# Kernel optimization log

Hardware: AMD Instinct MI355X
Metric: run time of the kernel (lower is better)

The kernel has to match this reference:

```python
import jax, jax.numpy as jnp
import numpy as np

B, SEQ, NNODES = 4, 12, 1024
SEG_LEN, SEG_NUM = 3, 4
HID, FF, DK, NH, NLAYERS = 64, 2048, 32, 8, 2


def setup_inputs() -> dict:
    key = jax.random.key(0)
    ks = iter(jax.random.split(key, 64))
    def nrm(shape, scale=0.05):
        return jax.random.normal(next(ks), shape, dtype=jnp.float32) * scale
    ones = lambda s: jnp.ones(s, jnp.float32)
    zeros = lambda s: jnp.zeros(s, jnp.float32)
    S, L = 2, NLAYERS
    return {
        'traffic': nrm((B, SEQ, NNODES), 1.0),
        'user': nrm((B, SEQ, NNODES), 1.0),
        'patch_w': nrm((S, HID, SEG_LEN)), 'patch_b': nrm((S, HID)),
        'mha_w': nrm((S, L, 3 * HID, HID)), 'mha_b': nrm((S, L, 3 * HID)),
        'out_w': nrm((S, L, HID, HID)), 'out_b': nrm((S, L, HID)),
        'ff1_w': nrm((S, L, FF, HID)), 'ff1_b': nrm((S, L, FF)),
        'ff2_w': nrm((S, L, HID, FF)), 'ff2_b': nrm((S, L, HID)),
        'ln1_g': ones((S, L, HID)), 'ln1_b': zeros((S, L, HID)),
        'ln2_g': ones((S, L, HID)), 'ln2_b': zeros((S, L, HID)),
        'ga_wq': nrm((S, L, DK, HID)), 'ga_wk': nrm((S, L, DK, HID)), 'ga_wv': nrm((S, L, HID, HID)),
        'ga_ff1_w': nrm((S, L, FF, HID)), 'ga_ff1_b': nrm((S, L, FF)),
        'ga_ff2_w': nrm((S, L, HID, FF)), 'ga_ff2_b': nrm((S, L, HID)),
        'ga_ln1_g': ones((S, L, HID)), 'ga_ln1_b': zeros((S, L, HID)),
        'ga_ln2_g': ones((S, L, HID)), 'ga_ln2_b': zeros((S, L, HID)),
        'ca_wq': nrm((DK, 2 * HID)), 'ca_wk': nrm((DK, 2 * HID)), 'ca_wv': nrm((HID, 2 * HID)),
    }


def _ln(x, g, b, eps=1e-5):
    m = x.mean(-1, keepdims=True)
    v = jnp.mean((x - m) ** 2, -1, keepdims=True)
    return (x - m) / jnp.sqrt(v + eps) * g + b


def _pe(s, d):
    pos = jnp.arange(s, dtype=jnp.float32)[:, None]
    div = jnp.exp(jnp.arange(0, d, 2, dtype=jnp.float32) * (-np.log(10000.0) / d))
    pe = jnp.zeros((s, d), jnp.float32)
    pe = pe.at[:, 0::2].set(jnp.sin(pos * div))
    pe = pe.at[:, 1::2].set(jnp.cos(pos * div))
    return pe


def _mha(x, w, b, wo, bo):
    # standard nn.MultiheadAttention self-attn, batch_first; x: [B,S,H]
    qkv = x @ w.T + b
    q, k, v = jnp.split(qkv, 3, axis=-1)
    def heads(t):
        b_, s_, h_ = t.shape
        return t.reshape(b_, s_, NH, h_ // NH).transpose(0, 2, 1, 3)
    q, k, v = heads(q), heads(k), heads(v)
    scale = 1.0 / jnp.sqrt(jnp.float32(HID // NH))
    att = jax.nn.softmax(jnp.einsum('bhqd,bhkd->bhqk', q, k) * scale, axis=-1)
    o = jnp.einsum('bhqk,bhkd->bhqd', att, v).transpose(0, 2, 1, 3).reshape(x.shape)
    return o @ wo.T + bo


def _enc_layer(x, p):
    # TransformerEncoderLayer_cross, post-norm, dropout=0 (eval)
    x = _ln(x + _mha(x, p['mw'], p['mb'], p['ow'], p['ob']), p['g1'], p['b1'])
    f = jax.nn.relu(x @ p['f1w'].T + p['f1b']) @ p['f2w'].T + p['f2b']
    return _ln(x + f, p['g2'], p['b2'])


def _graph_att(x, p):
    # GraphAttention.forward (bias=None, mask=None, dropout=0)
    q = x @ p['wq'].T
    k = x @ p['wk'].T
    v = x @ p['wv'].T
    dist = jax.nn.softmax(jnp.einsum('bnd,bmd->bnm', q, k) / jnp.sqrt(jnp.float32(DK)), axis=-1)
    att = jnp.einsum('bnm,bmd->bnd', dist, v)
    att = _ln(att, p['g1'], p['b1']) + x
    f = jax.nn.relu(att @ p['f1w'].T + p['f1b']) @ p['f2w'].T + p['f2b']
    return _ln(att + f, p['g2'], p['b2'])


def reference(traffic, user, patch_w, patch_b, mha_w, mha_b, out_w, out_b,
              ff1_w, ff1_b, ff2_w, ff2_b, ln1_g, ln1_b, ln2_g, ln2_b,
              ga_wq, ga_wk, ga_wv, ga_ff1_w, ga_ff1_b, ga_ff2_w, ga_ff2_b,
              ga_ln1_g, ga_ln1_b, ga_ln2_g, ga_ln2_b, ca_wq, ca_wk, ca_wv):
    pe = _pe(SEG_NUM, HID)

    def encode(x, s):
        b, _, d = x.shape
        # DSW_embedding: b (seg_num seg_len) d -> b d seg_num seg_len, then Linear
        seg = x.reshape(b, SEG_NUM, SEG_LEN, d).transpose(0, 3, 1, 2)
        z = seg @ patch_w[s].T + patch_b[s]          # [b, d, seg_num, HID]
        z = z + pe                                    # positional encoding over patches
        for i in range(NLAYERS):
            # temporal attention over the patch axis
            zt = z.reshape(b * d, SEG_NUM, HID)
            zt = _enc_layer(zt, dict(mw=mha_w[s, i], mb=mha_b[s, i], ow=out_w[s, i], ob=out_b[s, i],
                                     f1w=ff1_w[s, i], f1b=ff1_b[s, i], f2w=ff2_w[s, i], f2b=ff2_b[s, i],
                                     g1=ln1_g[s, i], b1=ln1_b[s, i], g2=ln2_g[s, i], b2=ln2_b[s, i]))
            z = zt.reshape(b, d, SEG_NUM, HID)
            # spatial graph attention over the node axis
            zs = z.transpose(0, 2, 1, 3).reshape(b * SEG_NUM, d, HID)
            zs = _graph_att(zs, dict(wq=ga_wq[s, i], wk=ga_wk[s, i], wv=ga_wv[s, i],
                                     f1w=ga_ff1_w[s, i], f1b=ga_ff1_b[s, i], f2w=ga_ff2_w[s, i], f2b=ga_ff2_b[s, i],
                                     g1=ga_ln1_g[s, i], b1=ga_ln1_b[s, i], g2=ga_ln2_g[s, i], b2=ga_ln2_b[s, i]))
            z = zs.reshape(b, SEG_NUM, d, HID).transpose(0, 2, 1, 3)
        return z.mean(axis=2)                         # pool patches -> [b, d, HID]

    enc = jnp.concatenate([encode(traffic, 0), encode(user, 1)], axis=-1)  # [b, d, 2*HID]
    # encoder_attn: SelfAttention(2*HID -> dim_k=32, dim_v=HID)
    q = enc @ ca_wq.T
    k = enc @ ca_wk.T
    v = enc @ ca_wv.T
    dist = jax.nn.softmax(jnp.einsum('bnd,bmd->bnm', q, k) / jnp.sqrt(jnp.float32(DK)), axis=-1)
    return jnp.einsum('bnm,bmd->bnd', dist, v)        # [b, n_nodes, HID]
```

## Files before the change

kernel.cpp:

```cpp
#include <hip/hip_runtime.h>
#include <hip/hip_bf16.h>
#include <math.h>

#define BB 4
#define SEQL 12
#define NN 1024
#define SEGL 3
#define SEGN 4
#define HID 64
#define FFD 2048
#define DKK 32
#define NHH 8
#define HDD 8
#define ZS 1048576

using bf16 = __hip_bfloat16;
__device__ __forceinline__ float b2f(bf16 v) { return __bfloat162float(v); }

typedef __attribute__((ext_vector_type(8))) short s8v;
typedef __attribute__((ext_vector_type(4))) float f4v;
typedef __attribute__((ext_vector_type(4))) unsigned short u4v;

__device__ __forceinline__ unsigned short f2b(float f) {
  bf16 h = __float2bfloat16(f);
  unsigned short u; __builtin_memcpy(&u, &h, 2); return u;
}
__device__ __forceinline__ float us2f(unsigned short u) {
  unsigned int e = ((unsigned int)u) << 16;
  float f; __builtin_memcpy(&f, &e, 4); return f;
}

template <int F>
__device__ __forceinline__ float ldw(const void* p, long i) {
  if (F) return ((const float*)p)[i];
  return b2f(((const bf16*)p)[i]);
}
template <int F>
__device__ __forceinline__ s8v ldfrag(const void* p, long elemOff) {
  if (F) {
    const float* fp = (const float*)p + elemOff;
    f4v u = *(const f4v*)fp, v = *(const f4v*)(fp + 4);
    s8v t;
    t[0]=f2b(u[0]); t[1]=f2b(u[1]); t[2]=f2b(u[2]); t[3]=f2b(u[3]);
    t[4]=f2b(v[0]); t[5]=f2b(v[1]); t[6]=f2b(v[2]); t[7]=f2b(v[3]);
    return t;
  }
  return *(const s8v*)((const unsigned short*)p + elemOff);
}
template <int F>
__device__ __forceinline__ f4v ldb4(const void* p, long i) {
  if (F) return *(const f4v*)((const float*)p + i);
  u4v u = *(const u4v*)((const unsigned short*)p + i);
  f4v r; r[0]=us2f(u[0]); r[1]=us2f(u[1]); r[2]=us2f(u[2]); r[3]=us2f(u[3]);
  return r;
}

__global__ void k_zero(unsigned short* __restrict__ o, int n) {
  int i = blockIdx.x * 256 + threadIdx.x;
  if (i < n) o[i] = 0;
}

__global__ void k_detect(const void* __restrict__ x0, int* __restrict__ flag) {
  int t = threadIdx.x;
  int bad = 0;
  const bf16* p = (const bf16*)x0;
  for (int i = t; i < 512; i += 256) {
    float a = fabsf(b2f(p[i]));
    if (!(a < 1e4f) || (a != 0.f && a < 1e-4f)) bad = 1;
  }
  __shared__ int tot;
  if (t == 0) tot = 0;
  __syncthreads();
  unsigned long long m = __ballot(bad);
  if ((t & 63) == 0) atomicAdd(&tot, __popcll(m));
  __syncthreads();
  if (t == 0) *flag = (tot > 64) ? 1 : 0;
}

template <int F>
__device__ __forceinline__ void wconv_body(const void* __restrict__ w1,
    const void* __restrict__ w2, const void* __restrict__ w3,
    const void* __restrict__ w4, unsigned short* __restrict__ out) {
  int i = blockIdx.x * 256 + threadIdx.x;
  long e8 = (long)i * 8;
  int slot = (int)(e8 >> 17);
  int si = slot >> 2, which = slot & 3;
  long r = e8 & 131071;
  const void* src = (which == 0) ? w1 : (which == 1) ? w2 : (which == 2) ? w3 : w4;
  *(s8v*)(out + e8) = ldfrag<F>(src, (long)si*FFD*HID + r);
}
__global__ __launch_bounds__(256) void k_wconv(const void* w1, const void* w2,
    const void* w3, const void* w4, unsigned short* out,
    const int* __restrict__ flag) {
  if (*flag) wconv_body<1>(w1, w2, w3, w4, out);
  else       wconv_body<0>(w1, w2, w3, w4, out);
}

template <int F>
__device__ __forceinline__ void patch_body(const void* __restrict__ xt,
    const void* __restrict__ xu,
    const void* __restrict__ pw, const void* __restrict__ pb,
    float* __restrict__ z) {
  int bid = blockIdx.x;
  int s = bid >> 12, rem = bid & 4095;
  int b = rem >> 10, n = rem & 1023;
  const void* x = s ? xu : xt;
  long opw = (long)s*HID*SEGL, opb = (long)s*HID;
  int g = threadIdx.x >> 6, h = threadIdx.x & 63;
  float acc = ldw<F>(pb, opb + h);
#pragma unroll
  for (int l = 0; l < SEGL; ++l)
    acc += ldw<F>(x, (long)(b*SEQL + g*SEGL + l)*NN + n) * ldw<F>(pw, opw + h*SEGL + l);
  int i2 = h >> 1;
  float dv = expf((float)(2*i2) * (-logf(10000.f) / (float)HID));
  float ang = (float)g * dv;
  acc += (h & 1) ? cosf(ang) : sinf(ang);
  z[(long)s*ZS + ((long)(b*NN + n)*SEGN + g)*HID + h] = acc;
}
__global__ __launch_bounds__(256) void k_patch(const void* __restrict__ xt,
    const void* __restrict__ xu,
    const void* __restrict__ pw, const void* __restrict__ pb,
    float* __restrict__ z, const int* __restrict__ flag) {
  if (*flag) patch_body<1>(xt, xu, pw, pb, z);
  else       patch_body<0>(xt, xu, pw, pb, z);
}

#define TT 64
#define FRW 64
#define HCS 74

__device__ __forceinline__ void ff_ld(const unsigned short* __restrict__ wc1,
    const unsigned short* __restrict__ wc2, int hb, int srow, int le,
    s8v* r1, s8v* r2) {
  r1[0] = *(const s8v*)(wc1 + (long)(hb + srow)*HID + le*8);
  r1[1] = *(const s8v*)(wc1 + (long)(hb + srow + 8)*HID + le*8);
  r2[0] = *(const s8v*)(wc2 + (long)srow*FFD + hb + le*8);
  r2[1] = *(const s8v*)(wc2 + (long)(srow + 8)*FFD + hb + le*8);
}
__device__ __forceinline__ void ff_wr(char* ldsbuf, int pb, int srow, int swb,
    const s8v* r1, const s8v* r2) {
  char* w1b = ldsbuf + pb*8192;
  char* w2b = ldsbuf + 16384 + pb*8192;
  *(s8v*)(w1b + srow*128 + swb) = r1[0];
  *(s8v*)(w1b + (srow + 8)*128 + swb) = r1[1];
  *(s8v*)(w2b + srow*128 + swb) = r2[0];
  *(s8v*)(w2b + (srow + 8)*128 + swb) = r2[1];
}

template <int F>
__device__ __forceinline__ void tff_body(float* __restrict__ zb,
    const void* __restrict__ W, const void* __restrict__ bq,
    const void* __restrict__ WO, const void* __restrict__ bo,
    const void* __restrict__ g1, const void* __restrict__ b1,
    const unsigned short* __restrict__ wcw, int li,
    const void* __restrict__ B1, const void* __restrict__ B2,
    const void* __restrict__ G, const void* __restrict__ Bt,
    char* lds) {
  int s = blockIdx.x >> 8, blk = blockIdx.x & 255;
  long si = s*2 + li;
  float* z = zb + (long)s*ZS;
  long oW = si*3*HID*HID, obq = si*3*HID, oWO = si*HID*HID, obo = si*HID;
  long og1 = si*HID, ob1 = si*HID;
  const unsigned short* wc1 = wcw + (si*4 + 0)*131072;
  const unsigned short* wc2 = wcw + (si*4 + 1)*131072;
  long fob1 = si*FFD, fob2 = si*HID, fog = si*HID, fobt = si*HID;
  unsigned short (*qkvs)[200] = (unsigned short(*)[200])lds;
  unsigned short (*ao)[72]    = (unsigned short(*)[72])(lds + 25600);
  float (*yb)[68]             = (float(*)[68])(lds + 34816);
  int tid = threadIdx.x;
  int w = tid >> 6, lane = tid & 63;
  int col = lane & 15, quad = lane >> 4;
  long r0 = (long)blk * TT;
  float* stashW = (float*)(lds + 59648 + w*4352);

  int lr = lane >> 3, le = lane & 7;
  int srow = w*16 + lr;
  int swb = ((le ^ lr) << 4);
  s8v cw1[2], cw2[2];
  ff_ld(wc1, wc2, 0, srow, le, cw1, cw2);

  s8v bx[4][2];
#pragma unroll
  for (int mt = 0; mt < 4; ++mt) {
    const float* xr = z + (r0 + mt*16 + col) * HID;
#pragma unroll
    for (int ks = 0; ks < 2; ++ks) {
      const float* p = xr + ks*32 + quad*8;
      f4v u = *(const f4v*)p, v = *(const f4v*)(p + 4);
      s8v t;
      t[0]=f2b(u[0]); t[1]=f2b(u[1]); t[2]=f2b(u[2]); t[3]=f2b(u[3]);
      t[4]=f2b(v[0]); t[5]=f2b(v[1]); t[6]=f2b(v[2]); t[7]=f2b(v[3]);
      bx[mt][ks] = t;
    }
  }
#pragma unroll
  for (int nt = 0; nt < 3; ++nt) {
    int cbase = (w*3 + nt) * 16;
    s8v aw[2];
#pragma unroll
    for (int ks = 0; ks < 2; ++ks)
      aw[ks] = ldfrag<F>(W, oW + (long)(cbase + col)*HID + ks*32 + quad*8);
    f4v bv = ldb4<F>(bq, obq + cbase + quad*4);
#pragma unroll
    for (int mt = 0; mt < 4; ++mt) {
      f4v sv = (f4v){0.f,0.f,0.f,0.f};
#pragma unroll
      for (int ks = 0; ks < 2; ++ks)
        sv = __builtin_amdgcn_mfma_f32_16x16x32_bf16(aw[ks], bx[mt][ks], sv, 0, 0, 0);
      unsigned short pk[4];
#pragma unroll
      for (int r = 0; r < 4; ++r) pk[r] = f2b(sv[r] + bv[r]);
      *(unsigned long long*)&qkvs[mt*16 + col][cbase + quad*4] =
        (unsigned long long)pk[0] | ((unsigned long long)pk[1] << 16) |
        ((unsigned long long)pk[2] << 32) | ((unsigned long long)pk[3] << 48);
    }
  }
  __syncthreads();
  if (tid < 128) {
    int gi = tid >> 3, hd = tid & 7;
    int tl = gi * 4;
    float qv[4][8], kv[4][8], vv[4][8];
#pragma unroll
    for (int t4 = 0; t4 < 4; ++t4) {
      s8v qq = *(const s8v*)&qkvs[tl + t4][hd*8];
      s8v kk = *(const s8v*)&qkvs[tl + t4][64 + hd*8];
      s8v vq = *(const s8v*)&qkvs[tl + t4][128 + hd*8];
#pragma unroll
      for (int e = 0; e < 8; ++e) {
        qv[t4][e] = us2f((unsigned short)qq[e]);
        kv[t4][e] = us2f((unsigned short)kk[e]);
        vv[t4][e] = us2f((unsigned short)vq[e]);
      }
    }
    const float sc8 = 0.3535533905932738f;
#pragma unroll
    for (int qt = 0; qt < 4; ++qt) {
      float sc[4]; float mx = -1e30f;
#pragma unroll
      for (int kt = 0; kt < 4; ++kt) {
        float d = 0;
#pragma unroll
        for (int e = 0; e < 8; ++e) d += qv[qt][e]*kv[kt][e];
        sc[kt] = d*sc8; mx = fmaxf(mx, sc[kt]);
      }
      float se = 0;
#pragma unroll
      for (int kt = 0; kt < 4; ++kt) { sc[kt] = expf(sc[kt]-mx); se += sc[kt]; }
      float inv = 1.f/se;
      s8v outp;
#pragma unroll
      for (int e = 0; e < 8; ++e) {
        float o = 0;
#pragma unroll
        for (int kt = 0; kt < 4; ++kt) o += sc[kt]*vv[kt][e];
        outp[e] = (short)f2b(o*inv);
      }
      *(s8v*)&ao[tl + qt][hd*8] = outp;
    }
  }
  __syncthreads();
  s8v awo[2];
#pragma unroll
  for (int ks = 0; ks < 2; ++ks)
    awo[ks] = ldfrag<F>(WO, oWO + (long)(w*16 + col)*HID + ks*32 + quad*8);
  f4v bov = ldb4<F>(bo, obo + w*16 + quad*4);
#pragma unroll
  for (int mt = 0; mt < 4; ++mt) {
    f4v ov = (f4v){0.f,0.f,0.f,0.f};
#pragma unroll
    for (int ks = 0; ks < 2; ++ks) {
      s8v bao = *(const s8v*)&ao[mt*16 + col][ks*32 + quad*8];
      ov = __builtin_amdgcn_mfma_f32_16x16x32_bf16(awo[ks], bao, ov, 0, 0, 0);
    }
    f4v yv;
#pragma unroll
    for (int r = 0; r < 4; ++r) yv[r] = ov[r] + bov[r];
    *(f4v*)&yb[mt*16 + col][w*16 + quad*4] = yv;
  }
  __syncthreads();
  {
    float gg = ldw<F>(g1, og1 + lane), bb2 = ldw<F>(b1, ob1 + lane);
#pragma unroll
    for (int rr = 0; rr < 16; ++rr) {
      int row = w*16 + rr;
      long tok = r0 + row;
      float val = yb[row][lane] + z[tok*HID + lane];
      float sm = val;
#pragma unroll
      for (int off = 32; off; off >>= 1) sm += __shfl_xor(sm, off);
      float m = sm*(1.f/HID);
      float d = val - m, sq = d*d;
#pragma unroll
      for (int off = 32; off; off >>= 1) sq += __shfl_xor(sq, off);
      float rv = rsqrtf(sq*(1.f/HID) + 1e-5f);
      stashW[rr*68 + lane] = d*rv*gg + bb2;
    }
  }
  __syncthreads();

  unsigned short* hcw = (unsigned short*)(lds + 32768 + w*2368);
  float* red = (float*)(lds + 42240 + w*4352);

  s8v bx2[2];
#pragma unroll
  for (int ks = 0; ks < 2; ++ks) {
    const float* p = &stashW[col*68 + ks*32 + quad*8];
    f4v u = *(const f4v*)p, v = *(const f4v*)(p + 4);
    s8v t;
    t[0]=f2b(u[0]); t[1]=f2b(u[1]); t[2]=f2b(u[2]); t[3]=f2b(u[3]);
    t[4]=f2b(v[0]); t[5]=f2b(v[1]); t[6]=f2b(v[2]); t[7]=f2b(v[3]);
    bx2[ks] = t;
  }

  f4v acc[4];
#pragma unroll
  for (int m = 0; m < 4; ++m) acc[m] = (f4v){0.f,0.f,0.f,0.f};

  ff_wr(lds, 0, srow, swb, cw1, cw2);
  __syncthreads();

  const int sw = (col & 7) << 4;
  s8v nw1[2], nw2[2];
  for (int c = 0; c < 32; ++c) {
    int pb = c & 1;
    if (c < 31) ff_ld(wc1, wc2, (c+1)*64, srow, le, nw1, nw2);
    const char* w1b = lds + pb*8192;
    const char* w2b = lds + 16384 + pb*8192;
    const int hb = c*64;
#pragma unroll
    for (int t = 0; t < 4; ++t) {
      int row = t*16 + col;
      s8v a10 = *(const s8v*)(w1b + row*128 + ((quad*16) ^ sw));
      s8v a11 = *(const s8v*)(w1b + row*128 + ((64 + quad*16) ^ sw));
      f4v bv = ldb4<F>(B1, fob1 + hb + t*16 + quad*4);
      f4v sv = __builtin_amdgcn_mfma_f32_16x16x32_bf16(a10, bx2[0],
                 (f4v){0.f,0.f,0.f,0.f}, 0, 0, 0);
      sv = __builtin_amdgcn_mfma_f32_16x16x32_bf16(a11, bx2[1], sv, 0, 0, 0);
      unsigned short pk[4];
#pragma unroll
      for (int r = 0; r < 4; ++r) pk[r] = f2b(fmaxf(sv[r] + bv[r], 0.f));
      *(unsigned long long*)&hcw[col*HCS + t*16 + quad*4] =
        (unsigned long long)pk[0] | ((unsigned long long)pk[1] << 16) |
        ((unsigned long long)pk[2] << 32) | ((unsigned long long)pk[3] << 48);
    }
#pragma unroll
    for (int ks2 = 0; ks2 < 2; ++ks2) {
      s8v bh = *(const s8v*)&hcw[col*HCS + ks2*32 + quad*8];
#pragma unroll
      for (int m = 0; m < 4; ++m) {
        int r2 = m*16 + col;
        s8v a2 = *(const s8v*)(w2b + r2*128 + ((ks2*64 + quad*16) ^ sw));
        acc[m] = __builtin_amdgcn_mfma_f32_16x16x32_bf16(a2, bh, acc[m], 0, 0, 0);
      }
    }
    if (c < 31) ff_wr(lds, pb ^ 1, srow, swb, nw1, nw2);
    __syncthreads();
  }

#pragma unroll
  for (int m = 0; m < 4; ++m)
    *(f4v*)&red[col*68 + m*16 + quad*4] = acc[m];
  float fgg = ldw<F>(G, fog + lane), fbbt = ldw<F>(Bt, fobt + lane);
  float b2v = ldw<F>(B2, fob2 + lane);
#pragma unroll
  for (int rr = 0; rr < 16; ++rr) {
    long grow = r0 + w*16 + rr;
    float val = red[rr*68 + lane] + b2v + stashW[rr*68 + lane];
    float sm = val;
#pragma unroll
    for (int off = 32; off; off >>= 1) sm += __shfl_xor(sm, off);
    float m = sm * (1.f/HID);
    float d = val - m;
    float sq = d*d;
#pragma unroll
    for (int off = 32; off; off >>= 1) sq += __shfl_xor(sq, off);
    float rv = rsqrtf(sq*(1.f/HID) + 1e-5f);
    z[grow*HID + lane] = d*rv*fgg + fbbt;
  }
}
__global__ __launch_bounds__(256) void k_tff(float* __restrict__ z,
    const void* W, const void* bqkv, const void* WO, const void* bo,
    const void* g1, const void* b1,
    const unsigned short* __restrict__ wcw, int li,
    const void* B1, const void* B2, const void* G, const void* Bt,
    const int* __restrict__ flag) {
  __shared__ __attribute__((aligned(16))) char lds[77056];
  if (*flag) tff_body<1>(z, W, bqkv, WO, bo, g1, b1, wcw, li, B1, B2, G, Bt, lds);
  else       tff_body<0>(z, W, bqkv, WO, bo, g1, b1, wcw, li, B1, B2, G, Bt, lds);
}

template <int F>
__device__ __forceinline__ void ffmfma_body(float* __restrict__ xb,
    const unsigned short* __restrict__ wcw, int li, int wsel,
    const void* __restrict__ B1, const void* __restrict__ B2,
    const void* __restrict__ G, const void* __restrict__ Bt,
    float* __restrict__ enc, int dop,
    char* ldsbuf) {
  int s = blockIdx.x >> 8, blk = blockIdx.x & 255;
  long si = s*2 + li;
  float* x = xb + (long)s*ZS;
  const unsigned short* wc1 = wcw + (si*4 + wsel)*131072;
  const unsigned short* wc2 = wcw + (si*4 + wsel + 1)*131072;
  long ob1 = si*FFD, ob2 = si*HID, og = si*HID, obt = si*HID;
  int tid = threadIdx.x;
  int w = tid >> 6, lane = tid & 63;
  int col = lane & 15, quad = lane >> 4;
  long r0 = (long)blk * FRW;
  unsigned short* hcw = (unsigned short*)(ldsbuf + 32768 + w*2368);
  float* red = (float*)(ldsbuf + 42240 + w*4352);

  long tokc = r0 + w*16 + col;
  s8v bx[2];
  {
    const float* xr = x + tokc * HID;
#pragma unroll
    for (int ks = 0; ks < 2; ++ks) {
      const float* p = xr + ks*32 + quad*8;
      f4v u = *(const f4v*)p, v = *(const f4v*)(p + 4);
      s8v t;
      t[0]=f2b(u[0]); t[1]=f2b(u[1]); t[2]=f2b(u[2]); t[3]=f2b(u[3]);
      t[4]=f2b(v[0]); t[5]=f2b(v[1]); t[6]=f2b(v[2]); t[7]=f2b(v[3]);
      bx[ks] = t;
    }
  }

  int lr = lane >> 3;
  int le = lane & 7;
  int srow = w*16 + lr;
  int swb = ((le ^ lr) << 4);

  f4v acc[4];
#pragma unroll
  for (int m = 0; m < 4; ++m) acc[m] = (f4v){0.f,0.f,0.f,0.f};

  s8v cw1[2], cw2[2], nw1[2], nw2[2];
  ff_ld(wc1, wc2, 0, srow, le, cw1, cw2);
  ff_wr(ldsbuf, 0, srow, swb, cw1, cw2);
  __syncthreads();

  const int sw = (col & 7) << 4;
  for (int c = 0; c < 32; ++c) {
    int pb = c & 1;
    if (c < 31) ff_ld(wc1, wc2, (c+1)*64, srow, le, nw1, nw2);
    const char* w1b = ldsbuf + pb*8192;
    const char* w2b = ldsbuf + 16384 + pb*8192;
    const int hb = c*64;
#pragma unroll
    for (int t = 0; t < 4; ++t) {
      int row = t*16 + col;
      s8v a10 = *(const s8v*)(w1b + row*128 + ((quad*16) ^ sw));
      s8v a11 = *(const s8v*)(w1b + row*128 + ((64 + quad*16) ^ sw));
      f4v bv = ldb4<F>(B1, ob1 + hb + t*16 + quad*4);
      f4v sv = __builtin_amdgcn_mfma_f32_16x16x32_bf16(a10, bx[0],
                 (f4v){0.f,0.f,0.f,0.f}, 0, 0, 0);
      sv = __builtin_amdgcn_mfma_f32_16x16x32_bf16(a11, bx[1], sv, 0, 0, 0);
      unsigned short pk[4];
#pragma unroll
      for (int r = 0; r < 4; ++r) pk[r] = f2b(fmaxf(sv[r] + bv[r], 0.f));
      *(unsigned long long*)&hcw[col*HCS + t*16 + quad*4] =
        (unsigned long long)pk[0] | ((unsigned long long)pk[1] << 16) |
        ((unsigned long long)pk[2] << 32) | ((unsigned long long)pk[3] << 48);
    }
#pragma unroll
    for (int ks2 = 0; ks2 < 2; ++ks2) {
      s8v bh = *(const s8v*)&hcw[col*HCS + ks2*32 + quad*8];
#pragma unroll
      for (int m = 0; m < 4; ++m) {
        int r2 = m*16 + col;
        s8v a2 = *(const s8v*)(w2b + r2*128 + ((ks2*64 + quad*16) ^ sw));
        acc[m] = __builtin_amdgcn_mfma_f32_16x16x32_bf16(a2, bh, acc[m], 0, 0, 0);
      }
    }
    if (c < 31) ff_wr(ldsbuf, pb ^ 1, srow, swb, nw1, nw2);
    __syncthreads();
  }

#pragma unroll
  for (int m = 0; m < 4; ++m)
    *(f4v*)&red[col*68 + m*16 + quad*4] = acc[m];
  float gg = ldw<F>(G, og + lane), bbt = ldw<F>(Bt, obt + lane);
  float b2v = ldw<F>(B2, ob2 + lane);
  float pacc[4] = {0.f,0.f,0.f,0.f};
#pragma unroll
  for (int rr = 0; rr < 16; ++rr) {
    long grow = r0 + w*16 + rr;
    float val = red[rr*68 + lane] + b2v + x[grow*HID + lane];
    float sm = val;
#pragma unroll
    for (int off = 32; off; off >>= 1) sm += __shfl_xor(sm, off);
    float m = sm * (1.f/HID);
    float d = val - m;
    float sq = d*d;
#pragma unroll
    for (int off = 32; off; off >>= 1) sq += __shfl_xor(sq, off);
    float rv = rsqrtf(sq*(1.f/HID) + 1e-5f);
    float fin = d*rv*gg + bbt;
    x[grow*HID + lane] = fin;
    pacc[rr >> 2] += fin;
  }
  if (dop) {
#pragma unroll
    for (int j = 0; j < 4; ++j) {
      long tok = r0 + w*16 + j*4;
      enc[(tok >> 2)*(2*HID) + s*HID + lane] = pacc[j]*0.25f;
    }
  }
}
__global__ __launch_bounds__(256) void k_ffmfma(float* __restrict__ x,
    const unsigned short* __restrict__ wcw, int li, int wsel,
    const void* B1, const void* B2, const void* G, const void* Bt,
    float* enc, int dop, const int* __restrict__ flag) {
  __shared__ __attribute__((aligned(16))) char ldsbuf[59648];
  if (*flag) ffmfma_body<1>(x, wcw, li, wsel, B1, B2, G, Bt, enc, dop, ldsbuf);
  else       ffmfma_body<0>(x, wcw, li, wsel, B1, B2, G, Bt, enc, dop, ldsbuf);
}

template <int F>
__device__ __forceinline__ void gqkv_body(const float* __restrict__ zb,
    const void* __restrict__ wq, const void* __restrict__ wk,
    const void* __restrict__ wv, int li,
    unsigned short* __restrict__ q, unsigned short* __restrict__ k,
    unsigned short* __restrict__ vt) {
  int tid = threadIdx.x;
  int w = tid >> 6, lane = tid & 63;
  int col = lane & 15, quad = lane >> 4;
  int sg = blockIdx.x >> 4;
  int s = sg >> 4, bg = sg & 15;
  int n0 = (blockIdx.x & 15) * 64;
  int b = bg >> 2, g = bg & 3;
  long si = s*2 + li;
  const float* z = zb + (long)s*ZS;
  long oq = si*DKK*HID, ok = si*DKK*HID, ov = si*HID*HID;
  long gbase = (long)sg * NN;

  s8v bx[4][2];
#pragma unroll
  for (int rt = 0; rt < 4; ++rt) {
    const float* xr = z + ((long)(b*NN + n0 + rt*16 + col)*SEGN + g)*HID;
#pragma unroll
    for (int ks = 0; ks < 2; ++ks) {
      const float* p = xr + ks*32 + quad*8;
      f4v u = *(const f4v*)p, vv = *(const f4v*)(p + 4);
      s8v t;
      t[0]=f2b(u[0]); t[1]=f2b(u[1]); t[2]=f2b(u[2]); t[3]=f2b(u[3]);
      t[4]=f2b(vv[0]); t[5]=f2b(vv[1]); t[6]=f2b(vv[2]); t[7]=f2b(vv[3]);
      bx[rt][ks] = t;
    }
  }

#pragma unroll
  for (int tt = 0; tt < 2; ++tt) {
    int ct = w*2 + tt;
    const void* wp; long wo; int co; int kind;
    if (ct < 2)      { wp = wq; wo = oq; co = ct*16;      kind = 0; }
    else if (ct < 4) { wp = wk; wo = ok; co = (ct-2)*16;  kind = 1; }
    else             { wp = wv; wo = ov; co = (ct-4)*16;  kind = 2; }
    s8v aw[2];
#pragma unroll
    for (int ks = 0; ks < 2; ++ks)
      aw[ks] = ldfrag<F>(wp, wo + (long)(co + col)*HID + ks*32 + quad*8);
#pragma unroll
    for (int rt = 0; rt < 4; ++rt) {
      f4v sv = (f4v){0.f,0.f,0.f,0.f};
#pragma unroll
      for (int ks = 0; ks < 2; ++ks)
        sv = __builtin_amdgcn_mfma_f32_16x16x32_bf16(aw[ks], bx[rt][ks], sv, 0, 0, 0);
      int key = n0 + rt*16 + col;
      if (kind == 2) {
        long vbase = (long)sg*HID*NN;
#pragma unroll
        for (int r = 0; r < 4; ++r)
          vt[vbase + (long)(co + quad*4 + r)*NN + key] = f2b(sv[r]);
      } else {
        long row = gbase + key;
        unsigned short pk[4];
#pragma unroll
        for (int r = 0; r < 4; ++r) pk[r] = f2b(sv[r]);
        unsigned short* dst = kind ? k : q;
        *(unsigned long long*)&dst[row*DKK + co + quad*4] =
          (unsigned long long)pk[0] | ((unsigned long long)pk[1] << 16) |
          ((unsigned long long)pk[2] << 32) | ((unsigned long long)pk[3] << 48);
      }
    }
  }
}
__global__ __launch_bounds__(256) void k_gqkv(const float* __restrict__ z,
    const void* wq, const void* wk, const void* wv, int li,
    unsigned short* q, unsigned short* k, unsigned short* vt,
    const int* __restrict__ flag) {
  if (*flag) gqkv_body<1>(z, wq, wk, wv, li, q, k, vt);
  else       gqkv_body<0>(z, wq, wk, wv, li, q, k, vt);
}

__global__ __launch_bounds__(512) void k_gattn(float* __restrict__ zb,
    const unsigned short* __restrict__ qb, const unsigned short* __restrict__ kb,
    const unsigned short* __restrict__ vtb,
    const void* __restrict__ g1, const void* __restrict__ b1, int li,
    const int* __restrict__ flag) {
  int f = *flag;
  __shared__ unsigned short pl[2][8][16][74];
  __shared__ float accb[8][16][66];
  __shared__ float lb[8][16];
  int tid = threadIdx.x;
  int w = tid >> 6, lane = tid & 63;
  int col = lane & 15, quad = lane >> 4;
  int qt = w >> 1, kh = w & 1;
  int sg = blockIdx.x >> 4;
  int s = sg >> 4, bg = sg & 15;
  int n0 = (blockIdx.x & 15) * 64;
  long si = s*2 + li;
  float* z = zb + (long)s*ZS;
  long og1 = si*HID, ob1 = si*HID;
  long gbase = (long)sg * NN;
  const unsigned short* vrow = vtb + (long)sg*HID*NN;

  s8v aq = *(const s8v*)(qb + (gbase + n0 + qt*16 + col)*DKK + quad*8);

  f4v acc[4];
#pragma unroll
  for (int t = 0; t < 4; ++t) acc[t] = (f4v){0.f,0.f,0.f,0.f};
  float psum[4] = {0.f,0.f,0.f,0.f};
  const float rs = 0.17677669529663687f;
  const int cbeg = kh * 512;

#pragma unroll 2
  for (int it = 0; it < 8; ++it) {
    int c0 = cbeg + it*64;
    int pb = it & 1;
    f4v s4[4];
#pragma unroll
    for (int nt = 0; nt < 4; ++nt) {
      s8v bk = *(const s8v*)(kb + (gbase + c0 + nt*16 + col)*DKK + quad*8);
      s4[nt] = __builtin_amdgcn_mfma_f32_16x16x32_bf16(aq, bk,
                (f4v){0.f,0.f,0.f,0.f}, 0, 0, 0);
    }
#pragma unroll
    for (int r = 0; r < 4; ++r) {
      float p0 = expf(s4[0][r]*rs), p1 = expf(s4[1][r]*rs);
      float p2 = expf(s4[2][r]*rs), p3 = expf(s4[3][r]*rs);
      psum[r] += (p0 + p1) + (p2 + p3);
      int row = quad*4 + r;
      pl[pb][w][row][col]      = f2b(p0);
      pl[pb][w][row][16 + col] = f2b(p1);
      pl[pb][w][row][32 + col] = f2b(p2);
      pl[pb][w][row][48 + col] = f2b(p3);
    }
#pragma unroll
    for (int ks = 0; ks < 2; ++ks) {
      s8v ap = *(const s8v*)&pl[pb][w][col][ks*32 + quad*8];
#pragma unroll
      for (int nt = 0; nt < 4; ++nt) {
        s8v bv = *(const s8v*)(vrow + (long)(nt*16 + col)*NN + c0 + ks*32 + quad*8);
        acc[nt] = __builtin_amdgcn_mfma_f32_16x16x32_bf16(ap, bv, acc[nt], 0, 0, 0);
      }
    }
  }

#pragma unroll
  for (int r = 0; r < 4; ++r) {
    float v = psum[r];
#pragma unroll
    for (int off = 1; off < 16; off <<= 1) v += __shfl_xor(v, off);
    psum[r] = v;
  }
#pragma unroll
  for (int t = 0; t < 4; ++t)
#pragma unroll
    for (int r = 0; r < 4; ++r)
      accb[w][quad*4 + r][t*16 + col] = acc[t][r];
  if (col == 0) {
#pragma unroll
    for (int r = 0; r < 4; ++r) lb[w][quad*4 + r] = psum[r];
  }
  __syncthreads();

  int b = bg >> 2, g = bg & 3;
  float gg = f ? ((const float*)g1)[og1 + lane] : b2f(((const bf16*)g1)[og1 + lane]);
  float bb = f ? ((const float*)b1)[ob1 + lane] : b2f(((const bf16*)b1)[ob1 + lane]);
#pragma unroll
  for (int rr = 0; rr < 8; ++rr) {
    int rl = w*8 + rr;
    int qtt = rl >> 4, lr = rl & 15;
    float a = accb[2*qtt][lr][lane] + accb[2*qtt + 1][lr][lane];
    float l = lb[2*qtt][lr] + lb[2*qtt + 1][lr];
    float val = a / l;
    float s2 = val;
#pragma unroll
    for (int off = 32; off; off >>= 1) s2 += __shfl_xor(s2, off);
    float m = s2*(1.f/HID);
    float d = val - m, sq = d*d;
#pragma unroll
    for (int off = 32; off; off >>= 1) sq += __shfl_xor(sq, off);
    float r = rsqrtf(sq*(1.f/HID) + 1e-5f);
    float* zp = z + ((long)(b*NN + n0 + rl)*SEGN + g)*HID;
    zp[lane] = d*r*gg + bb + zp[lane];
  }
}

template <int F>
__device__ __forceinline__ void fqkv_body(const float* __restrict__ enc,
    const void* __restrict__ wq, const void* __restrict__ wk,
    const void* __restrict__ wv,
    unsigned short* __restrict__ q, unsigned short* __restrict__ k,
    unsigned short* __restrict__ vt, float* xs) {
  long r = blockIdx.x;
  int t = threadIdx.x;
  xs[t] = enc[r*128 + t];
  __syncthreads();
  if (t < 32) {
    long wr = (long)t*128; float a = 0;
    for (int e = 0; e < 128; ++e) a += xs[e]*ldw<F>(wq, wr + e);
    q[r*DKK + t] = f2b(a);
  } else if (t < 64) {
    long wr = (long)(t-32)*128; float a = 0;
    for (int e = 0; e < 128; ++e) a += xs[e]*ldw<F>(wk, wr + e);
    k[r*DKK + (t-32)] = f2b(a);
  } else {
    long wr = (long)(t-64)*128; float a = 0;
    for (int e = 0; e < 128; ++e) a += xs[e]*ldw<F>(wv, wr + e);
    vt[((r >> 10)*HID + (t-64))*NN + (r & 1023)] = f2b(a);
  }
}
__global__ __launch_bounds__(128) void k_fqkv(const float* __restrict__ enc,
    const void* wq, const void* wk, const void* wv,
    unsigned short* q, unsigned short* k, unsigned short* vt,
    const int* __restrict__ flag) {
  __shared__ float xs[2*HID];
  if (*flag) fqkv_body<1>(enc, wq, wk, wv, q, k, vt, xs);
  else       fqkv_body<0>(enc, wq, wk, wv, q, k, vt, xs);
}

__global__ __launch_bounds__(512) void k_fattn(
    const unsigned short* __restrict__ qb, const unsigned short* __restrict__ kb,
    const unsigned short* __restrict__ vtb, void* __restrict__ outp,
    const int* __restrict__ flag) {
  __shared__ unsigned short pl[2][8][16][74];
  __shared__ float accb[8][16][66];
  __shared__ float lb[8][16];
  int tid = threadIdx.x;
  int w = tid >> 6, lane = tid & 63;
  int col = lane & 15, quad = lane >> 4;
  int qt = w >> 1, kh = w & 1;
  int b = blockIdx.x >> 4;
  int n0 = (blockIdx.x & 15) * 64;
  long gbase = (long)b * NN;
  const unsigned short* vrow = vtb + (long)b*HID*NN;

  s8v aq = *(const s8v*)(qb + (gbase + n0 + qt*16 + col)*DKK + quad*8);

  f4v acc[4];
#pragma unroll
  for (int t = 0; t < 4; ++t) acc[t] = (f4v){0.f,0.f,0.f,0.f};
  float psum[4] = {0.f,0.f,0.f,0.f};
  const float rs = 0.17677669529663687f;
  const int cbeg = kh * 512;

#pragma unroll 2
  for (int it = 0; it < 8; ++it) {
    int c0 = cbeg + it*64;
    int pb = it & 1;
    f4v s4[4];
#pragma unroll
    for (int nt = 0; nt < 4; ++nt) {
      s8v bk = *(const s8v*)(kb + (gbase + c0 + nt*16 + col)*DKK + quad*8);
      s4[nt] = __builtin_amdgcn_mfma_f32_16x16x32_bf16(aq, bk,
                (f4v){0.f,0.f,0.f,0.f}, 0, 0, 0);
    }
#pragma unroll
    for (int r = 0; r < 4; ++r) {
      float p0 = expf(s4[0][r]*rs), p1 = expf(s4[1][r]*rs);
      float p2 = expf(s4[2][r]*rs), p3 = expf(s4[3][r]*rs);
      psum[r] += (p0 + p1) + (p2 + p3);
      int row = quad*4 + r;
      pl[pb][w][row][col]      = f2b(p0);
      pl[pb][w][row][16 + col] = f2b(p1);
      pl[pb][w][row][32 + col] = f2b(p2);
      pl[pb][w][row][48 + col] = f2b(p3);
    }
#pragma unroll
    for (int ks = 0; ks < 2; ++ks) {
      s8v ap = *(const s8v*)&pl[pb][w][col][ks*32 + quad*8];
#pragma unroll
      for (int nt = 0; nt < 4; ++nt) {
        s8v bv = *(const s8v*)(vrow + (long)(nt*16 + col)*NN + c0 + ks*32 + quad*8);
        acc[nt] = __builtin_amdgcn_mfma_f32_16x16x32_bf16(ap, bv, acc[nt], 0, 0, 0);
      }
    }
  }

#pragma unroll
  for (int r = 0; r < 4; ++r) {
    float v = psum[r];
#pragma unroll
    for (int off = 1; off < 16; off <<= 1) v += __shfl_xor(v, off);
    psum[r] = v;
  }
#pragma unroll
  for (int t = 0; t < 4; ++t)
#pragma unroll
    for (int r = 0; r < 4; ++r)
      accb[w][quad*4 + r][t*16 + col] = acc[t][r];
  if (col == 0) {
#pragma unroll
    for (int r = 0; r < 4; ++r) lb[w][quad*4 + r] = psum[r];
  }
  __syncthreads();

  int f = *flag;
#pragma unroll
  for (int rr = 0; rr < 8; ++rr) {
    int rl = w*8 + rr;
    int qtt = rl >> 4, lr = rl & 15;
    float a = accb[2*qtt][lr][lane] + accb[2*qtt + 1][lr][lane];
    float l = lb[2*qtt][lr] + lb[2*qtt + 1][lr];
    float val = a / l;
    long idx = (gbase + n0 + rl)*HID + lane;
    if (f) ((float*)outp)[idx] = val;
    else   ((bf16*)outp)[idx] = __float2bfloat16(val);
  }
}

extern "C" void kernel_launch(void* const* d_in, const int* in_sizes, int n_in,
                              void* d_out, int out_size, void* d_ws, size_t ws_size,
                              hipStream_t stream) {
  static const int EXP[30] = {
    49152, 49152, 384, 128, 49152, 768, 16384, 256,
    524288, 8192, 524288, 256, 256, 256, 256, 256,
    8192, 8192, 16384, 524288, 8192, 524288, 256, 256,
    256, 256, 256, 4096, 4096, 8192
  };
  const size_t NEED = (size_t)(2*ZS + 524288 + 524288 + 524288 + 1048576 + 1048576) * 4 + 64;
  bool ok = (n_in == 30) && (ws_size >= NEED) && (out_size == BB*NN*HID);
  if (ok) for (int i = 0; i < 30; ++i) ok = ok && (in_sizes[i] == EXP[i]);
  if (!ok) {
    k_zero<<<(BB*NN*HID + 255)/256, 256, 0, stream>>>((unsigned short*)d_out, BB*NN*HID);
    return;
  }

  float* z   = (float*)d_ws;
  float* enc = z   + 2*ZS;
  float* qb  = enc + 524288;
  float* kb  = qb  + 524288;
  float* vb  = kb  + 524288;
  float* wcf = vb  + 1048576;
  int*  flag = (int*)(wcf + 1048576);
  unsigned short* wcw = (unsigned short*)wcf;

  k_detect<<<1, 256, 0, stream>>>(d_in[0], flag);

  const void *i_traffic=d_in[0], *i_user=d_in[1], *i_pw=d_in[2], *i_pb=d_in[3],
    *i_mw=d_in[4], *i_mb=d_in[5], *i_ow=d_in[6], *i_ob=d_in[7], *i_f1w=d_in[8],
    *i_f1b=d_in[9], *i_f2w=d_in[10], *i_f2b=d_in[11], *i_l1g=d_in[12],
    *i_l1b=d_in[13], *i_l2g=d_in[14], *i_l2b=d_in[15], *i_gwq=d_in[16],
    *i_gwk=d_in[17], *i_gwv=d_in[18], *i_gf1w=d_in[19], *i_gf1b=d_in[20],
    *i_gf2w=d_in[21], *i_gf2b=d_in[22], *i_gl1g=d_in[23], *i_gl1b=d_in[24],
    *i_gl2g=d_in[25], *i_gl2b=d_in[26], *i_cwq=d_in[27], *i_cwk=d_in[28],
    *i_cwv=d_in[29];

  k_wconv<<<1024, 256, 0, stream>>>(i_f1w, i_f2w, i_gf1w, i_gf2w, wcw, flag);
  k_patch<<<2*BB*NN, 256, 0, stream>>>(i_traffic, i_user, i_pw, i_pb, z, flag);

  for (int i = 0; i < 2; ++i) {
    k_tff<<<512, 256, 0, stream>>>(z, i_mw, i_mb, i_ow, i_ob,
        i_l1g, i_l1b, wcw, i, i_f1b, i_f2b, i_l2g, i_l2b, flag);
    k_gqkv<<<512, 256, 0, stream>>>(z, i_gwq, i_gwk, i_gwv, i,
        (unsigned short*)qb, (unsigned short*)kb, (unsigned short*)vb, flag);
    k_gattn<<<512, 512, 0, stream>>>(z,
        (const unsigned short*)qb, (const unsigned short*)kb,
        (const unsigned short*)vb, i_gl1g, i_gl1b, i, flag);
    k_ffmfma<<<512, 256, 0, stream>>>(z, wcw, i, 2,
        i_gf1b, i_gf2b, i_gl2g, i_gl2b, enc, (i == 1) ? 1 : 0, flag);
  }
  k_fqkv<<<BB*NN, 128, 0, stream>>>(enc, i_cwq, i_cwk, i_cwv,
      (unsigned short*)qb, (unsigned short*)kb, (unsigned short*)vb, flag);
  k_fattn<<<BB*16, 512, 0, stream>>>((const unsigned short*)qb,
      (const unsigned short*)kb, (unsigned short*)vb, d_out, flag);
}
```

Baseline: 601.4 us.

## Deepen FF weight prefetch to two chunks ahead and alias reduction LDS

```diff
diff --git a/kernel.cpp b/kernel.cpp
--- a/kernel.cpp
+++ b/kernel.cpp
@@ -145,6 +145,39 @@
   *(s8v*)(w1b + (srow + 8)*128 + swb) = r1[1];
   *(s8v*)(w2b + srow*128 + swb) = r2[0];
   *(s8v*)(w2b + (srow + 8)*128 + swb) = r2[1];
+}
+template <int F>
+__device__ __forceinline__ void ff_compute(const char* ldsbuf, int pb, int hb,
+    int col, int quad, int sw, const s8v* bx, unsigned short* hcw,
+    const void* __restrict__ B1, long ob1, f4v* acc) {
+  const char* w1b = ldsbuf + pb*8192;
+  const char* w2b = ldsbuf + 16384 + pb*8192;
+#pragma unroll
+  for (int t = 0; t < 4; ++t) {
+    int row = t*16 + col;
+    s8v a10 = *(const s8v*)(w1b + row*128 + ((quad*16) ^ sw));
+    s8v a11 = *(const s8v*)(w1b + row*128 + ((64 + quad*16) ^ sw));
+    f4v bv = ldb4<F>(B1, ob1 + hb + t*16 + quad*4);
+    f4v sv = __builtin_amdgcn_mfma_f32_16x16x32_bf16(a10, bx[0],
+               (f4v){0.f,0.f,0.f,0.f}, 0, 0, 0);
+    sv = __builtin_amdgcn_mfma_f32_16x16x32_bf16(a11, bx[1], sv, 0, 0, 0);
+    unsigned short pk[4];
+#pragma unroll
+    for (int r = 0; r < 4; ++r) pk[r] = f2b(fmaxf(sv[r] + bv[r], 0.f));
+    *(unsigned long long*)&hcw[col*HCS + t*16 + quad*4] =
+      (unsigned long long)pk[0] | ((unsigned long long)pk[1] << 16) |
+      ((unsigned long long)pk[2] << 32) | ((unsigned long long)pk[3] << 48);
+  }
+#pragma unroll
+  for (int ks2 = 0; ks2 < 2; ++ks2) {
+    s8v bh = *(const s8v*)&hcw[col*HCS + ks2*32 + quad*8];
+#pragma unroll
+    for (int m = 0; m < 4; ++m) {
+      int r2 = m*16 + col;
+      s8v a2 = *(const s8v*)(w2b + r2*128 + ((ks2*64 + quad*16) ^ sw));
+      acc[m] = __builtin_amdgcn_mfma_f32_16x16x32_bf16(a2, bh, acc[m], 0, 0, 0);
+    }
+  }
 }
 
 template <int F>
@@ -316,44 +349,21 @@
 #pragma unroll
   for (int m = 0; m < 4; ++m) acc[m] = (f4v){0.f,0.f,0.f,0.f};
 
+  s8v rA1[2], rA2[2], rB1[2], rB2[2];
+  ff_ld(wc1, wc2, 64, srow, le, rA1, rA2);
+  ff_ld(wc1, wc2, 128, srow, le, rB1, rB2);
   ff_wr(lds, 0, srow, swb, cw1, cw2);
   __syncthreads();
 
   const int sw = (col & 7) << 4;
-  s8v nw1[2], nw2[2];
-  for (int c = 0; c < 32; ++c) {
-    int pb = c & 1;
-    if (c < 31) ff_ld(wc1, wc2, (c+1)*64, srow, le, nw1, nw2);
-    const char* w1b = lds + pb*8192;
-    const char* w2b = lds + 16384 + pb*8192;
-    const int hb = c*64;
-#pragma unroll
-    for (int t = 0; t < 4; ++t) {
-      int row = t*16 + col;
-      s8v a10 = *(const s8v*)(w1b + row*128 + ((quad*16) ^ sw));
-      s8v a11 = *(const s8v*)(w1b + row*128 + ((64 + quad*16) ^ sw));
-      f4v bv = ldb4<F>(B1, fob1 + hb + t*16 + quad*4);
-      f4v sv = __builtin_amdgcn_mfma_f32_16x16x32_bf16(a10, bx2[0],
-                 (f4v){0.f,0.f,0.f,0.f}, 0, 0, 0);
-      sv = __builtin_amdgcn_mfma_f32_16x16x32_bf16(a11, bx2[1], sv, 0, 0, 0);
-      unsigned short pk[4];
-#pragma unroll
-      for (int r = 0; r < 4; ++r) pk[r] = f2b(fmaxf(sv[r] + bv[r], 0.f));
-      *(unsigned long long*)&hcw[col*HCS + t*16 + quad*4] =
-        (unsigned long long)pk[0] | ((unsigned long long)pk[1] << 16) |
-        ((unsigned long long)pk[2] << 32) | ((unsigned long long)pk[3] << 48);
-    }
-#pragma unroll
-    for (int ks2 = 0; ks2 < 2; ++ks2) {
-      s8v bh = *(const s8v*)&hcw[col*HCS + ks2*32 + quad*8];
-#pragma unroll
-      for (int m = 0; m < 4; ++m) {
-        int r2 = m*16 + col;
-        s8v a2 = *(const s8v*)(w2b + r2*128 + ((ks2*64 + quad*16) ^ sw));
-        acc[m] = __builtin_amdgcn_mfma_f32_16x16x32_bf16(a2, bh, acc[m], 0, 0, 0);
-      }
-    }
-    if (c < 31) ff_wr(lds, pb ^ 1, srow, swb, nw1, nw2);
+  for (int c = 0; c < 32; c += 2) {
+    ff_compute<F>(lds, 0, c*64, col, quad, sw, bx2, hcw, B1, fob1, acc);
+    ff_wr(lds, 1, srow, swb, rA1, rA2);
+    if (c + 3 < 32) ff_ld(wc1, wc2, (c+3)*64, srow, le, rA1, rA2);
+    __syncthreads();
+    ff_compute<F>(lds, 1, (c+1)*64, col, quad, sw, bx2, hcw, B1, fob1, acc);
+    if (c + 2 < 32) ff_wr(lds, 0, srow, swb, rB1, rB2);
+    if (c + 4 < 32) ff_ld(wc1, wc2, (c+4)*64, srow, le, rB1, rB2);
     __syncthreads();
   }
 
@@ -407,7 +417,7 @@
   int col = lane & 15, quad = lane >> 4;
   long r0 = (long)blk * FRW;
   unsigned short* hcw = (unsigned short*)(ldsbuf + 32768 + w*2368);
-  float* red = (float*)(ldsbuf + 42240 + w*4352);
+  float* red = (float*)(ldsbuf + w*4352);
 
   long tokc = r0 + w*16 + col;
   s8v bx[2];
@@ -433,45 +443,22 @@
 #pragma unroll
   for (int m = 0; m < 4; ++m) acc[m] = (f4v){0.f,0.f,0.f,0.f};
 
-  s8v cw1[2], cw2[2], nw1[2], nw2[2];
-  ff_ld(wc1, wc2, 0, srow, le, cw1, cw2);
-  ff_wr(ldsbuf, 0, srow, swb, cw1, cw2);
+  s8v t1[2], t2[2], rA1[2], rA2[2], rB1[2], rB2[2];
+  ff_ld(wc1, wc2, 0, srow, le, t1, t2);
+  ff_wr(ldsbuf, 0, srow, swb, t1, t2);
+  ff_ld(wc1, wc2, 64, srow, le, rA1, rA2);
+  ff_ld(wc1, wc2, 128, srow, le, rB1, rB2);
   __syncthreads();
 
   const int sw = (col & 7) << 4;
-  for (int c = 0; c < 32; ++c) {
-    int pb = c & 1;
-    if (c < 31) ff_ld(wc1, wc2, (c+1)*64, srow, le, nw1, nw2);
-    const char* w1b = ldsbuf + pb*8192;
-    const char* w2b = ldsbuf + 16384 + pb*8192;
-    const int hb = c*64;
-#pragma unroll
-    for (int t = 0; t < 4; ++t) {
-      int row = t*16 + col;
-      s8v a10 = *(const s8v*)(w1b + row*128 + ((quad*16) ^ sw));
-      s8v a11 = *(const s8v*)(w1b + row*128 + ((64 + quad*16) ^ sw));
-      f4v bv = ldb4<F>(B1, ob1 + hb + t*16 + quad*4);
-      f4v sv = __builtin_amdgcn_mfma_f32_16x16x32_bf16(a10, bx[0],
-                 (f4v){0.f,0.f,0.f,0.f}, 0, 0, 0);
-      sv = __builtin_amdgcn_mfma_f32_16x16x32_bf16(a11, bx[1], sv, 0, 0, 0);
-      unsigned short pk[4];
-#pragma unroll
-      for (int r = 0; r < 4; ++r) pk[r] = f2b(fmaxf(sv[r] + bv[r], 0.f));
-      *(unsigned long long*)&hcw[col*HCS + t*16 + quad*4] =
-        (unsigned long long)pk[0] | ((unsigned long long)pk[1] << 16) |
-        ((unsigned long long)pk[2] << 32) | ((unsigned long long)pk[3] << 48);
-    }
-#pragma unroll
-    for (int ks2 = 0; ks2 < 2; ++ks2) {
-      s8v bh = *(const s8v*)&hcw[col*HCS + ks2*32 + quad*8];
-#pragma unroll
-      for (int m = 0; m < 4; ++m) {
-        int r2 = m*16 + col;
-        s8v a2 = *(const s8v*)(w2b + r2*128 + ((ks2*64 + quad*16) ^ sw));
-        acc[m] = __builtin_amdgcn_mfma_f32_16x16x32_bf16(a2, bh, acc[m], 0, 0, 0);
-      }
-    }
-    if (c < 31) ff_wr(ldsbuf, pb ^ 1, srow, swb, nw1, nw2);
+  for (int c = 0; c < 32; c += 2) {
+    ff_compute<F>(ldsbuf, 0, c*64, col, quad, sw, bx, hcw, B1, ob1, acc);
+    ff_wr(ldsbuf, 1, srow, swb, rA1, rA2);
+    if (c + 3 < 32) ff_ld(wc1, wc2, (c+3)*64, srow, le, rA1, rA2);
+    __syncthreads();
+    ff_compute<F>(ldsbuf, 1, (c+1)*64, col, quad, sw, bx, hcw, B1, ob1, acc);
+    if (c + 2 < 32) ff_wr(ldsbuf, 0, srow, swb, rB1, rB2);
+    if (c + 4 < 32) ff_ld(wc1, wc2, (c+4)*64, srow, le, rB1, rB2);
     __syncthreads();
   }
 
@@ -510,7 +497,7 @@
     const unsigned short* __restrict__ wcw, int li, int wsel,
     const void* B1, const void* B2, const void* G, const void* Bt,
     float* enc, int dop, const int* __restrict__ flag) {
-  __shared__ __attribute__((aligned(16))) char ldsbuf[59648];
+  __shared__ __attribute__((aligned(16))) char ldsbuf[42240];
   if (*flag) ffmfma_body<1>(x, wcw, li, wsel, B1, B2, G, Bt, enc, dop, ldsbuf);
   else       ffmfma_body<0>(x, wcw, li, wsel, B1, B2, G, Bt, enc, dop, ldsbuf);
 }
```

Result: no change. 603.0 us (+0.3%).
